# Kernel tuning notes

Hardware: AMD Instinct MI355X
Metric: run time of the kernel (lower is better)

The kernel has to match this reference:

```python
import jax, jax.numpy as jnp
import numpy as np

NUM_ROWS = 1_000_000   # len(row_end_offsets) - 1
NUM_COLS = 1_000_000   # numel of the gathered dense vector x
NNZ = 32_000_000       # avg_degree 32 per row


def setup_inputs() -> dict:
    key = jax.random.key(0)
    k1, k2, k3, k4 = jax.random.split(key, 4)
    spmat_values = jax.random.normal(k1, (NNZ,), dtype=jnp.float32)
    x = jax.random.normal(k2, (NUM_COLS,), dtype=jnp.float32)
    col_idx = jax.random.randint(k3, (NNZ,), 0, NUM_COLS, dtype=jnp.int32)
    row_end_offsets = jnp.sort(
        jax.random.randint(k4, (NUM_ROWS + 1,), 0, NNZ, dtype=jnp.int32)
    )
    return {
        "spmat_values": spmat_values,
        "x": x,
        "col_idx": col_idx,
        "row_end_offsets": row_end_offsets,
    }


def reference(spmat_values, x, col_idx, row_end_offsets):
    """Merged CSR SpMV: out[r] = sum_{j in [off[r], off[r+1])} vals[j] * x[col_idx[j]]."""
    num_rows = row_end_offsets.shape[0] - 1
    nnz = spmat_values.shape[0]
    # Row id of each nonzero: the segment r with off[r] <= j < off[r+1].
    row_ids = jnp.searchsorted(
        row_end_offsets[1:], jnp.arange(nnz, dtype=jnp.int32), side="right"
    )
    # Gather per-selector values from the dense vector, fuse elementwise product.
    prod = spmat_values * x[col_idx]
    out = jax.ops.segment_sum(
        prod, row_ids, num_segments=num_rows, indices_are_sorted=True
    )
    return out
```

## Files before the change

kernel.cpp:

```cpp
#include <hip/hip_runtime.h>


#define LANES_PER_ROW 8

__global__ void spmv_csr_vector(const float* __restrict__ vals,
                                const float* __restrict__ x,
                                const int*   __restrict__ col,
                                const int*   __restrict__ off,
                                float*       __restrict__ out,
                                int num_rows) {
    const int tid     = blockIdx.x * blockDim.x + threadIdx.x;
    const int group   = tid / LANES_PER_ROW;
    const int lane    = tid & (LANES_PER_ROW - 1);
    const int ngroups = (gridDim.x * blockDim.x) / LANES_PER_ROW;

    for (int r = group; r < num_rows; r += ngroups) {
        const int start = (r == 0) ? 0 : off[r];
        const int end   = off[r + 1];

        float sum = 0.0f;
        for (int j = start + lane; j < end; j += LANES_PER_ROW) {
            sum += vals[j] * x[col[j]];
        }

        sum += __shfl_xor(sum, 1, 64);
        sum += __shfl_xor(sum, 2, 64);
        sum += __shfl_xor(sum, 4, 64);

        if (lane == 0) out[r] = sum;
    }
}

extern "C" void kernel_launch(void* const* d_in, const int* in_sizes, int n_in,
                              void* d_out, int out_size, void* d_ws, size_t ws_size,
                              hipStream_t stream) {
    const float* vals = (const float*)d_in[0];
    const float* x    = (const float*)d_in[1];
    const int*   col  = (const int*)d_in[2];
    const int*   off  = (const int*)d_in[3];
    float*       out  = (float*)d_out;

    const int num_rows = in_sizes[3] - 1;

    const int block = 256;
    long long total_threads = (long long)num_rows * LANES_PER_ROW;
    int grid = (int)((total_threads + block - 1) / block);
    if (grid > 65535 * 8) grid = 65535 * 8;

    spmv_csr_vector<<<grid, block, 0, stream>>>(vals, x, col, off, out, num_rows);
}
```

Before: 487.8 us.

## Split SpMV into a vectorized product pass and a segmented row-sum pass

Splits the work into two kernels when workspace allows. The first computes vals*x[col] with vectorized nontemporal loads and stores into a workspace buffer, and the second sums each row's contiguous products with 16 lanes per row. The aim is coalesced, row-independent streaming of the gather instead of row-divergent access. The cost is writing and rereading an extra 128 MB product array plus a second launch. If the workspace is too small, the original single-kernel path still runs.

Measured after the change: 515.4 us. +5.7%, slower.

```diff
diff --git a/kernel.cpp b/kernel.cpp
--- a/kernel.cpp
+++ b/kernel.cpp
@@ -1,8 +1,57 @@
 #include <hip/hip_runtime.h>
 
 
-#define LANES_PER_ROW 8
+typedef int   vint4   __attribute__((ext_vector_type(4)));
+typedef float vfloat4 __attribute__((ext_vector_type(4)));
 
+__global__ void spmv_prod(const float* __restrict__ vals,
+                          const float* __restrict__ x,
+                          const int*   __restrict__ col,
+                          float*       __restrict__ prod,
+                          int nnz) {
+    const int t = blockIdx.x * blockDim.x + threadIdx.x;
+    int j = t * 4;
+    if (j + 3 < nnz) {
+        vint4   c = __builtin_nontemporal_load((const vint4*)(col + j));
+        vfloat4 v = __builtin_nontemporal_load((const vfloat4*)(vals + j));
+        vfloat4 p;
+        p.x = v.x * x[c.x];
+        p.y = v.y * x[c.y];
+        p.z = v.z * x[c.z];
+        p.w = v.w * x[c.w];
+        __builtin_nontemporal_store(p, (vfloat4*)(prod + j));
+    } else {
+        for (; j < nnz; ++j) prod[j] = vals[j] * x[col[j]];
+    }
+}
+
+#define L2R 16
+
+__global__ void spmv_rowsum(const float* __restrict__ prod,
+                            const int*   __restrict__ off,
+                            float*       __restrict__ out,
+                            int num_rows) {
+    const int tid  = blockIdx.x * blockDim.x + threadIdx.x;
+    const int r    = tid / L2R;
+    const int lane = tid & (L2R - 1);
+    if (r >= num_rows) return;
+
+    const int start = (r == 0) ? 0 : off[r];
+    const int end   = off[r + 1];
+
+    float s = 0.0f;
+    for (int j = start + lane; j < end; j += L2R)
+        s += __builtin_nontemporal_load(prod + j);
+
+    s += __shfl_xor(s, 1);
+    s += __shfl_xor(s, 2);
+    s += __shfl_xor(s, 4);
+    s += __shfl_xor(s, 8);
+
+    if (lane == 0) out[r] = s;
+}
+
+#define FB_LANES 8
 __global__ void spmv_csr_vector(const float* __restrict__ vals,
                                 const float* __restrict__ x,
                                 const int*   __restrict__ col,
@@ -10,23 +59,18 @@
                                 float*       __restrict__ out,
                                 int num_rows) {
     const int tid     = blockIdx.x * blockDim.x + threadIdx.x;
-    const int group   = tid / LANES_PER_ROW;
-    const int lane    = tid & (LANES_PER_ROW - 1);
-    const int ngroups = (gridDim.x * blockDim.x) / LANES_PER_ROW;
-
+    const int group   = tid / FB_LANES;
+    const int lane    = tid & (FB_LANES - 1);
+    const int ngroups = (gridDim.x * blockDim.x) / FB_LANES;
     for (int r = group; r < num_rows; r += ngroups) {
         const int start = (r == 0) ? 0 : off[r];
         const int end   = off[r + 1];
-
         float sum = 0.0f;
-        for (int j = start + lane; j < end; j += LANES_PER_ROW) {
+        for (int j = start + lane; j < end; j += FB_LANES)
             sum += vals[j] * x[col[j]];
-        }
-
-        sum += __shfl_xor(sum, 1, 64);
-        sum += __shfl_xor(sum, 2, 64);
-        sum += __shfl_xor(sum, 4, 64);
-
+        sum += __shfl_xor(sum, 1);
+        sum += __shfl_xor(sum, 2);
+        sum += __shfl_xor(sum, 4);
         if (lane == 0) out[r] = sum;
     }
 }
@@ -40,12 +84,21 @@
     const int*   off  = (const int*)d_in[3];
     float*       out  = (float*)d_out;
 
+    const int nnz      = in_sizes[0];
     const int num_rows = in_sizes[3] - 1;
+    const int block    = 256;
 
-    const int block = 256;
-    long long total_threads = (long long)num_rows * LANES_PER_ROW;
-    int grid = (int)((total_threads + block - 1) / block);
-    if (grid > 65535 * 8) grid = 65535 * 8;
+    if (ws_size >= (size_t)nnz * sizeof(float)) {
+        float* prod = (float*)d_ws;
+        int grid1 = (nnz / 4 + block - 1) / block + 1;
+        spmv_prod<<<grid1, block, 0, stream>>>(vals, x, col, prod, nnz);
 
-    spmv_csr_vector<<<grid, block, 0, stream>>>(vals, x, col, off, out, num_rows);
+        long long t2 = (long long)num_rows * L2R;
+        int grid2 = (int)((t2 + block - 1) / block);
+        spmv_rowsum<<<grid2, block, 0, stream>>>(prod, off, out, num_rows);
+    } else {
+        long long t = (long long)num_rows * FB_LANES;
+        int grid = (int)((t + block - 1) / block);
+        spmv_csr_vector<<<grid, block, 0, stream>>>(vals, x, col, off, out, num_rows);
+    }
 }
```
